# Kernel tuning notes

Measured on AMD Instinct MI355X. Metric: run time of the kernel, lower is better.

## Reference

```python
import jax, jax.numpy as jnp
import numpy as np

INP_SIZE = 3072
HID = 1024
OUT = 768
N_RES = 2  # same block (shared weights) applied twice, as in the torch code
EPS = 1e-5


def _layernorm(x, g, b):
    m = jnp.mean(x, axis=-1, keepdims=True)
    v = jnp.mean((x - m) ** 2, axis=-1, keepdims=True)
    return (x - m) / jnp.sqrt(v + EPS) * g + b


def setup_inputs() -> dict:
    key = jax.random.key(0)
    ks = jax.random.split(key, 8)
    bsz = 8192
    s = 0.02
    return {
        "inp": jax.random.normal(ks[0], (bsz, INP_SIZE), dtype=jnp.float32),
        "y": jax.random.normal(ks[1], (bsz, OUT), dtype=jnp.float32),
        "ln1_g": jnp.ones((INP_SIZE,), jnp.float32),
        "ln1_b": jnp.zeros((INP_SIZE,), jnp.float32),
        "W1": jax.random.normal(ks[2], (INP_SIZE, HID), dtype=jnp.float32) * s,
        "b1": jnp.zeros((HID,), jnp.float32),
        "Wa": jax.random.normal(ks[3], (HID, HID), dtype=jnp.float32) * s,
        "ba": jnp.zeros((HID,), jnp.float32),
        "Wb": jax.random.normal(ks[4], (HID, HID), dtype=jnp.float32) * s,
        "bb": jnp.zeros((HID,), jnp.float32),
        "W2": jax.random.normal(ks[5], (HID, OUT), dtype=jnp.float32) * s,
        "b2": jnp.zeros((OUT,), jnp.float32),
        "ln2_g": jnp.ones((OUT,), jnp.float32),
        "ln2_b": jnp.zeros((OUT,), jnp.float32),
    }


def reference(inp, y, ln1_g, ln1_b, W1, b1, Wa, ba, Wb, bb, W2, b2, ln2_g, ln2_b):
    bsz = inp.shape[0]
    # backbone (dropout in eval mode = identity)
    h = _layernorm(inp, ln1_g, ln1_b) @ W1 + b1  # [bsz, HID]
    for _ in range(N_RES):  # shared block weights, applied twice
        r = jax.nn.relu(jax.nn.relu(h @ Wa + ba) @ Wb + bb)
        h = h + r
    pred_y = _layernorm(h @ W2 + b2, ln2_g, ln2_b)  # [bsz, OUT]

    # batched contrastive cosine-sim loss (replaces per-sample python loop)
    pn = pred_y / jnp.linalg.norm(pred_y, axis=1, keepdims=True)
    yn = y / jnp.linalg.norm(y, axis=1, keepdims=True)
    S = pn @ yn.T  # [bsz, bsz] cosine similarities
    loss = -jnp.sum(pn * yn) + jnp.sum(jax.nn.logsumexp(S, axis=1))

    acc = jnp.mean((jnp.argmax(S, axis=1) == jnp.arange(bsz)).astype(jnp.float32))
    return pred_y, loss, acc
```

## Files before the change

### kernel.cpp

```cpp
#include <hip/hip_runtime.h>
#include <hip/hip_fp16.h>
#include <cstdint>
#include <math.h>

#define INP  3072
#define HID  1024
#define OUTD 768
#define BSZ  8192

typedef _Float16 f16;
typedef _Float16 f16x8 __attribute__((ext_vector_type(8)));
typedef _Float16 f16x4 __attribute__((ext_vector_type(4)));
typedef float    f32x4 __attribute__((ext_vector_type(4)));
typedef int      i32x4 __attribute__((ext_vector_type(4)));
typedef signed char s8;

static constexpr float LOG2E = 1.44269504088896340736f;
static constexpr float LN2   = 0.69314718055994530942f;
static constexpr float QS    = 384.0f;
static constexpr float CSC   = LOG2E / (QS * QS);

static constexpr size_t OFF_XH   = 0;
static constexpr size_t OFF_PN   = 0;
static constexpr size_t OFF_YN   = OFF_PN   + (size_t)BSZ*OUTD;
static constexpr size_t OFF_PSUM = OFF_YN   + (size_t)BSZ*OUTD;
static constexpr size_t OFF_PMAX = OFF_PSUM + (size_t)BSZ*64*4;
static constexpr size_t OFF_HB   = OFF_XH   + (size_t)BSZ*INP*2;
static constexpr size_t OFF_TT   = OFF_HB   + (size_t)BSZ*HID*2;
static constexpr size_t OFF_W1T  = OFF_TT   + (size_t)BSZ*OUTD*4;
static constexpr size_t OFF_WAT  = OFF_W1T  + (size_t)INP*HID*2;
static constexpr size_t OFF_WBT  = OFF_WAT  + (size_t)HID*HID*2;
static constexpr size_t OFF_W2T  = OFF_WBT  + (size_t)HID*HID*2;
static constexpr size_t OFF_DIAG = OFF_W2T  + (size_t)HID*OUTD*2;
static constexpr size_t OFF_ACC  = OFF_DIAG + (size_t)BSZ*4;

#define GL2LDS(gp, lp) __builtin_amdgcn_global_load_lds( \
    (__attribute__((address_space(1))) void*)(uintptr_t)(gp), \
    (__attribute__((address_space(3))) void*)(unsigned)(uintptr_t)(lp), 16, 0, 0)

__device__ __forceinline__ float blk_sum256(float v, float* sm) {
  #pragma unroll
  for (int d = 1; d < 64; d <<= 1) v += __shfl_xor(v, d, 64);
  int tid = threadIdx.x;
  __syncthreads();
  if ((tid & 63) == 0) sm[tid >> 6] = v;
  __syncthreads();
  return sm[0] + sm[1] + sm[2] + sm[3];
}

__device__ __forceinline__ s8 q8(float v) {
  int q = __float2int_rn(v * QS);
  q = q > 127 ? 127 : (q < -127 ? -127 : q);
  return (s8)q;
}

__global__ __launch_bounds__(256) void ln1_kernel(const float* __restrict__ inp,
    const float* __restrict__ g, const float* __restrict__ b, f16* __restrict__ xh) {
  __shared__ float sm[4];
  const int row = blockIdx.x, tid = threadIdx.x;
  const float4* x4 = (const float4*)(inp + (size_t)row * INP);
  float4 v[3]; float s = 0.f;
  #pragma unroll
  for (int i = 0; i < 3; i++) { v[i] = x4[tid + i*256]; s += v[i].x+v[i].y+v[i].z+v[i].w; }
  const float mean = blk_sum256(s, sm) * (1.f/INP);
  float s2 = 0.f;
  #pragma unroll
  for (int i = 0; i < 3; i++) {
    float dx=v[i].x-mean, dy=v[i].y-mean, dz=v[i].z-mean, dw=v[i].w-mean;
    s2 += dx*dx+dy*dy+dz*dz+dw*dw;
  }
  const float rstd = rsqrtf(blk_sum256(s2, sm) * (1.f/INP) + 1e-5f);
  const float4* g4p = (const float4*)g;
  const float4* b4p = (const float4*)b;
  f16x4* o4 = (f16x4*)(xh + (size_t)row * INP);
  #pragma unroll
  for (int i = 0; i < 3; i++) {
    const int c = tid + i*256;
    const float4 gg = g4p[c], bb = b4p[c];
    f16x4 t;
    t[0] = (f16)((v[i].x-mean)*rstd*gg.x + bb.x);
    t[1] = (f16)((v[i].y-mean)*rstd*gg.y + bb.y);
    t[2] = (f16)((v[i].z-mean)*rstd*gg.z + bb.z);
    t[3] = (f16)((v[i].w-mean)*rstd*gg.w + bb.w);
    o4[c] = t;
  }
}

__global__ __launch_bounds__(256) void transpose_all(
    const float* __restrict__ W1, const float* __restrict__ Wa,
    const float* __restrict__ Wb, const float* __restrict__ W2,
    f16* __restrict__ W1T, f16* __restrict__ WAT,
    f16* __restrict__ WBT, f16* __restrict__ W2T) {
  __shared__ float t[32][33];
  const int bI = blockIdx.x;
  const float* W; f16* Wt; int K, N, n0, k0;
  if (bI < 3072)      { int tt = bI;      W = W1; Wt = W1T; K = INP; N = HID;  n0 = (tt & 31)*32; k0 = (tt >> 5)*32; }
  else if (bI < 4096) { int tt = bI-3072; W = Wa; Wt = WAT; K = HID; N = HID;  n0 = (tt & 31)*32; k0 = (tt >> 5)*32; }
  else if (bI < 5120) { int tt = bI-4096; W = Wb; Wt = WBT; K = HID; N = HID;  n0 = (tt & 31)*32; k0 = (tt >> 5)*32; }
  else                { int tt = bI-5120; W = W2; Wt = W2T; K = HID; N = OUTD; int kq = tt/24; n0 = (tt - kq*24)*32; k0 = kq*32; }
  const int tx = threadIdx.x & 31, ty = threadIdx.x >> 5;
  #pragma unroll
  for (int i = 0; i < 32; i += 8) t[ty+i][tx] = W[(size_t)(k0+ty+i)*N + n0+tx];
  __syncthreads();
  #pragma unroll
  for (int i = 0; i < 32; i += 8) Wt[(size_t)(n0+ty+i)*K + k0+tx] = (f16)t[tx][ty+i];
}

__global__ __launch_bounds__(256) void ln2_yn(const float* __restrict__ pre,
    const float* __restrict__ g, const float* __restrict__ b,
    const float* __restrict__ y,
    float* __restrict__ outY, s8* __restrict__ pn, s8* __restrict__ yn) {
  __shared__ float sm[4];
  const int tid = threadIdx.x;
  if ((int)blockIdx.x < BSZ) {
    const int row = blockIdx.x;
    const float* x = pre + (size_t)row * OUTD;
    float v[3]; float s = 0.f;
    #pragma unroll
    for (int i = 0; i < 3; i++) { v[i] = x[tid + i*256]; s += v[i]; }
    const float mean = blk_sum256(s, sm) * (1.f/OUTD);
    float s2 = 0.f;
    #pragma unroll
    for (int i = 0; i < 3; i++) { float d = v[i]-mean; s2 += d*d; }
    const float rstd = rsqrtf(blk_sum256(s2, sm) * (1.f/OUTD) + 1e-5f);
    float z[3]; float n2 = 0.f;
    #pragma unroll
    for (int i = 0; i < 3; i++) { int c = tid + i*256; z[i] = (v[i]-mean)*rstd*g[c] + b[c]; n2 += z[i]*z[i]; }
    const float rn = rsqrtf(blk_sum256(n2, sm));
    float* oy = outY + (size_t)row * OUTD;
    s8*   op = pn   + (size_t)row * OUTD;
    #pragma unroll
    for (int i = 0; i < 3; i++) { int c = tid + i*256; oy[c] = z[i]; op[c] = q8(z[i]*rn); }
  } else {
    const int row = blockIdx.x - BSZ;
    const float* x = y + (size_t)row * OUTD;
    float v[3]; float n2 = 0.f;
    #pragma unroll
    for (int i = 0; i < 3; i++) { v[i] = x[tid + i*256]; n2 += v[i]*v[i]; }
    const float rn = rsqrtf(blk_sum256(n2, sm));
    s8* o = yn + (size_t)row * OUTD;
    #pragma unroll
    for (int i = 0; i < 3; i++) { int c = tid + i*256; o[c] = q8(v[i]*rn); }
  }
}

#define EPI_H   0
#define EPI_T   1
#define EPI_RES 2
#define EPI_P   3

template<int EPI>
__global__ __launch_bounds__(256) void gemm_bt(
    const f16* __restrict__ A, const f16* __restrict__ B, int K, int N,
    const float* __restrict__ bias, float* __restrict__ Cf, f16* __restrict__ Ch,
    const f16* __restrict__ Hin)
{
  __shared__ alignas(16) f16 lA[2][128*32];
  __shared__ alignas(16) f16 lB[2][128*32];
  const int tid  = threadIdx.x;
  const int wave = tid >> 6, lane = tid & 63;
  const int m0 = blockIdx.x * 128, n0 = blockIdx.y * 128;
  const int srow  = tid >> 2;
  const int skc   = tid & 3;
  const int skc_sw = skc ^ ((srow >> 1) & 3);
  const f16* gA = A + (size_t)(m0 + srow) * K + skc_sw*8;
  const f16* gB = B + (size_t)(n0 + srow) * K + skc_sw*8;
  const int wm = wave & 1, wn = wave >> 1;
  const int fm = lane & 15;
  const int g4 = lane >> 4;
  const int ks = (fm >> 1) & 3;
  const int ck = ((g4 ^ ks) * 8);

  f32x4 acc[4][4];
  #pragma unroll
  for (int i = 0; i < 4; i++)
    #pragma unroll
    for (int j = 0; j < 4; j++) acc[i][j] = (f32x4){0.f,0.f,0.f,0.f};

  const int iters = K >> 5;
  auto stage = [&](int buf, int k0) {
    f16* lAw = &lA[buf][wave*16*32];
    f16* lBw = &lB[buf][wave*16*32];
    GL2LDS(gA + k0,                lAw);
    GL2LDS(gA + (size_t)64*K + k0, lAw + 64*32);
    GL2LDS(gB + k0,                lBw);
    GL2LDS(gB + (size_t)64*K + k0, lBw + 64*32);
  };

  stage(0, 0);
  __syncthreads();
  for (int it = 0; it < iters; ++it) {
    const int cur = it & 1;
    if (it + 1 < iters) stage(cur ^ 1, (it + 1) << 5);
    f16x8 af[4], bf[4];
    #pragma unroll
    for (int i = 0; i < 4; i++) af[i] = *(const f16x8*)&lA[cur][(wm*64 + i*16 + fm)*32 + ck];
    #pragma unroll
    for (int j = 0; j < 4; j++) bf[j] = *(const f16x8*)&lB[cur][(wn*64 + j*16 + fm)*32 + ck];
    #pragma unroll
    for (int i = 0; i < 4; i++)
      #pragma unroll
      for (int j = 0; j < 4; j++)
        acc[i][j] = __builtin_amdgcn_mfma_f32_16x16x32_f16(af[i], bf[j], acc[i][j], 0, 0, 0);
    __syncthreads();
  }

  const int colb = n0 + wn*64;
  const int rowb = m0 + wm*64;
  #pragma unroll
  for (int i = 0; i < 4; i++) {
    #pragma unroll
    for (int j = 0; j < 4; j++) {
      const int col = colb + j*16 + fm;
      const float bs = bias[col];
      #pragma unroll
      for (int r = 0; r < 4; r++) {
        const int row = rowb + i*16 + g4*4 + r;
        float v = acc[i][j][r] + bs;
        const size_t idx = (size_t)row * N + col;
        if constexpr (EPI == EPI_H)        { Ch[idx] = (f16)v; }
        else if constexpr (EPI == EPI_T)   { v = fmaxf(v, 0.f); Ch[idx] = (f16)v; }
        else if constexpr (EPI == EPI_RES) { v = fmaxf(v, 0.f); v += (float)Hin[idx]; Ch[idx] = (f16)v; }
        else                               { Cf[idx] = v; }
      }
    }
  }
}

__global__ __launch_bounds__(256) void gemm_s8(
    const s8* __restrict__ A, const s8* __restrict__ B,
    float* __restrict__ partsum, float* __restrict__ partmax, float* __restrict__ diagv)
{
  __shared__ alignas(16) s8 lA[2][128*64];
  __shared__ alignas(16) s8 lB[2][128*64];
  __shared__ float redS[2][128], redM[2][128];
  const int K = OUTD;
  const int tid = threadIdx.x;
  const int wave = tid >> 6, lane = tid & 63;
  const int m0 = blockIdx.x * 128, n0 = blockIdx.y * 128;
  const int srow = tid >> 2;
  const int cl   = tid & 3;
  const int cg   = cl ^ ((srow ^ (srow >> 2)) & 3);
  const s8* gA = A + (size_t)(m0 + srow) * K + cg*16;
  const s8* gB = B + (size_t)(n0 + srow) * K + cg*16;
  const int wm = wave & 1, wn = wave >> 1;
  const int fm = lane & 15;
  const int g4 = lane >> 4;
  const int ksw = (fm ^ (fm >> 2)) & 3;
  const int ck8 = (g4 ^ ksw) * 16;

  i32x4 acc[4][4];
  #pragma unroll
  for (int i = 0; i < 4; i++)
    #pragma unroll
    for (int j = 0; j < 4; j++) acc[i][j] = (i32x4){0,0,0,0};

  auto stage = [&](int buf, int k0) {
    s8* lAw = &lA[buf][wave*16*64];
    s8* lBw = &lB[buf][wave*16*64];
    GL2LDS(gA + k0,                lAw);
    GL2LDS(gA + (size_t)64*K + k0, lAw + 64*64);
    GL2LDS(gB + k0,                lBw);
    GL2LDS(gB + (size_t)64*K + k0, lBw + 64*64);
  };

  stage(0, 0);
  __syncthreads();
  const int iters = K / 64;
  for (int it = 0; it < iters; ++it) {
    const int cur = it & 1;
    if (it + 1 < iters) stage(cur ^ 1, (it + 1) * 64);
    i32x4 af[4], bf[4];
    #pragma unroll
    for (int i = 0; i < 4; i++) af[i] = *(const i32x4*)&lA[cur][(wm*64 + i*16 + fm)*64 + ck8];
    #pragma unroll
    for (int j = 0; j < 4; j++) bf[j] = *(const i32x4*)&lB[cur][(wn*64 + j*16 + fm)*64 + ck8];
    #pragma unroll
    for (int i = 0; i < 4; i++)
      #pragma unroll
      for (int j = 0; j < 4; j++)
        acc[i][j] = __builtin_amdgcn_mfma_i32_16x16x64_i8(af[i], bf[j], acc[i][j], 0, 0, 0);
    __syncthreads();
  }

  if (m0 == n0) {
    #pragma unroll
    for (int i = 0; i < 4; i++)
      #pragma unroll
      for (int j = 0; j < 4; j++) {
        const int col = n0 + wn*64 + j*16 + fm;
        #pragma unroll
        for (int r = 0; r < 4; r++) {
          const int row = m0 + wm*64 + i*16 + g4*4 + r;
          if (row == col) diagv[row] = (float)acc[i][j][r] * CSC;
        }
      }
  }
  #pragma unroll
  for (int i = 0; i < 4; i++) {
    #pragma unroll
    for (int r = 0; r < 4; r++) {
      const float a0 = (float)acc[i][0][r] * CSC;
      const float a1 = (float)acc[i][1][r] * CSC;
      const float a2 = (float)acc[i][2][r] * CSC;
      const float a3 = (float)acc[i][3][r] * CSC;
      float s  = exp2f(a0) + exp2f(a1) + exp2f(a2) + exp2f(a3);
      float mx = fmaxf(fmaxf(a0, a1), fmaxf(a2, a3));
      #pragma unroll
      for (int d = 1; d < 16; d <<= 1) {
        s  += __shfl_xor(s, d, 64);
        mx  = fmaxf(mx, __shfl_xor(mx, d, 64));
      }
      if (fm == 0) { const int lrow = wm*64 + i*16 + g4*4 + r; redS[wn][lrow] = s; redM[wn][lrow] = mx; }
    }
  }
  __syncthreads();
  if (tid < 128) {
    const float sa = redS[0][tid] + redS[1][tid];
    const float ma = fmaxf(redM[0][tid], redM[1][tid]);
    const size_t p = (size_t)blockIdx.y * BSZ + m0 + tid;
    partsum[p] = sa; partmax[p] = ma;
  }
}

__global__ __launch_bounds__(256) void reduce_rows(const float* __restrict__ partsum,
    const float* __restrict__ partmax, const float* __restrict__ diagv,
    float* __restrict__ accum, float* __restrict__ out) {
  __shared__ float sm[4];
  const int row = blockIdx.x*256 + threadIdx.x;
  float s = 0.f, mx = -1e30f;
  for (int i = 0; i < 64; i++) {
    s  += partsum[(size_t)i*BSZ + row];
    mx  = fmaxf(mx, partmax[(size_t)i*BSZ + row]);
  }
  const float dgs  = diagv[row];
  const float corr = (dgs >= mx) ? 1.f : 0.f;
  const float lse  = logf(s);
  const float dg   = dgs * LN2;
  const float lse_s = blk_sum256(lse, sm);
  const float dg_s  = blk_sum256(dg, sm);
  const float c_s   = blk_sum256(corr, sm);
  if (threadIdx.x == 0) {
    atomicAdd(&accum[0], lse_s);
    atomicAdd(&accum[1], dg_s);
    atomicAdd(&accum[2], c_s);
    __threadfence();
    const unsigned old = atomicAdd((unsigned*)&accum[3], 1u);
    if (old == gridDim.x - 1) {
      const float a0 = atomicAdd(&accum[0], 0.f);
      const float a1 = atomicAdd(&accum[1], 0.f);
      const float a2 = atomicAdd(&accum[2], 0.f);
      out[0] = a0 - a1;
      out[1] = a2 * (1.f / BSZ);
    }
  }
}

extern "C" void kernel_launch(void* const* d_in, const int* in_sizes, int n_in,
                              void* d_out, int out_size, void* d_ws, size_t ws_size,
                              hipStream_t stream) {
  const float* inp  = (const float*)d_in[0];
  const float* y    = (const float*)d_in[1];
  const float* ln1g = (const float*)d_in[2];
  const float* ln1b = (const float*)d_in[3];
  const float* W1   = (const float*)d_in[4];
  const float* b1   = (const float*)d_in[5];
  const float* Wa   = (const float*)d_in[6];
  const float* ba   = (const float*)d_in[7];
  const float* Wb   = (const float*)d_in[8];
  const float* bb   = (const float*)d_in[9];
  const float* W2   = (const float*)d_in[10];
  const float* b2   = (const float*)d_in[11];
  const float* ln2g = (const float*)d_in[12];
  const float* ln2b = (const float*)d_in[13];
  float* out = (float*)d_out;

  char* ws = (char*)d_ws;
  f16*   XH   = (f16*)  (ws + OFF_XH);
  s8*    PN   = (s8*)   (ws + OFF_PN);
  s8*    YN   = (s8*)   (ws + OFF_YN);
  float* PSUM = (float*)(ws + OFF_PSUM);
  float* PMAX = (float*)(ws + OFF_PMAX);
  f16*   HB   = (f16*)  (ws + OFF_HB);
  f16*   T    = (f16*)  (ws + OFF_TT);
  float* PRE2 = (float*)(ws + OFF_TT);
  f16*   W1T  = (f16*)  (ws + OFF_W1T);
  f16*   WAT  = (f16*)  (ws + OFF_WAT);
  f16*   WBT  = (f16*)  (ws + OFF_WBT);
  f16*   W2T  = (f16*)  (ws + OFF_W2T);
  float* DIAG = (float*)(ws + OFF_DIAG);
  float* ACC  = (float*)(ws + OFF_ACC);

  transpose_all<<<5888, 256, 0, stream>>>(W1, Wa, Wb, W2, W1T, WAT, WBT, W2T);
  ln1_kernel<<<BSZ, 256, 0, stream>>>(inp, ln1g, ln1b, XH);

  gemm_bt<EPI_H><<<dim3(BSZ/128, HID/128), 256, 0, stream>>>(
      XH, W1T, INP, HID, b1, nullptr, HB, nullptr);

  for (int it = 0; it < 2; it++) {
    gemm_bt<EPI_T><<<dim3(BSZ/128, HID/128), 256, 0, stream>>>(
        HB, WAT, HID, HID, ba, nullptr, T, nullptr);
    gemm_bt<EPI_RES><<<dim3(BSZ/128, HID/128), 256, 0, stream>>>(
        T, WBT, HID, HID, bb, nullptr, HB, HB);
  }

  gemm_bt<EPI_P><<<dim3(BSZ/128, OUTD/128), 256, 0, stream>>>(
      HB, W2T, HID, OUTD, b2, PRE2, nullptr, nullptr);

  ln2_yn<<<2*BSZ, 256, 0, stream>>>(PRE2, ln2g, ln2b, y, out, PN, YN);

  hipMemsetAsync(ACC, 0, 4*sizeof(float), stream);

  gemm_s8<<<dim3(BSZ/128, BSZ/128), 256, 0, stream>>>(PN, YN, PSUM, PMAX, DIAG);

  reduce_rows<<<BSZ/256, 256, 0, stream>>>(PSUM, PMAX, DIAG, ACC, out + (size_t)BSZ*OUTD);
}
```

Before: 497.0 us.

## Pre-pack weights and int8 operands into MFMA fragment layout, load B directly to registers

Weights are transposed into an MFMA-fragment-packed layout, and the normalized int8 pred and target matrices are written in a packed 16-row tile layout. The GEMMs can then load B fragments (and both operands in the int8 similarity GEMM) straight from global memory into registers, bypassing LDS. The f16 GEMM now stages only A through LDS with a K=64 step and a new swizzle, and its grid axes are swapped. The int8 GEMM drops LDS staging entirely and remaps blocks so each XCD shares N tiles. This cuts LDS traffic and barriers, but relies on L2/cache hits for the direct global fragment loads, which are not coalesced the same way.

Result: slower. 543.9 us (+9.4%).

```diff
diff --git a/kernel.cpp b/kernel.cpp
--- a/kernel.cpp
+++ b/kernel.cpp
@@ -34,6 +34,7 @@
 static constexpr size_t OFF_DIAG = OFF_W2T  + (size_t)HID*OUTD*2;
 static constexpr size_t OFF_ACC  = OFF_DIAG + (size_t)BSZ*4;
 
+
 #define GL2LDS(gp, lp) __builtin_amdgcn_global_load_lds( \
     (__attribute__((address_space(1))) void*)(uintptr_t)(gp), \
     (__attribute__((address_space(3))) void*)(unsigned)(uintptr_t)(lp), 16, 0, 0)
@@ -86,7 +87,7 @@
   }
 }
 
-__global__ __launch_bounds__(256) void transpose_all(
+__global__ __launch_bounds__(256) void transpose_pack(
     const float* __restrict__ W1, const float* __restrict__ Wa,
     const float* __restrict__ Wb, const float* __restrict__ W2,
     f16* __restrict__ W1T, f16* __restrict__ WAT,
@@ -102,8 +103,17 @@
   #pragma unroll
   for (int i = 0; i < 32; i += 8) t[ty+i][tx] = W[(size_t)(k0+ty+i)*N + n0+tx];
   __syncthreads();
-  #pragma unroll
-  for (int i = 0; i < 32; i += 8) Wt[(size_t)(n0+ty+i)*K + k0+tx] = (f16)t[tx][ty+i];
+  const int tid = threadIdx.x;
+  if (tid < 128) {
+    const int fm = tid & 15, half = (tid >> 4) & 1, kc = tid >> 5;
+    const int n_l = half*16 + fm;
+    f16x8 v;
+    #pragma unroll
+    for (int e = 0; e < 8; e++) v[e] = (f16)t[kc*8 + e][n_l];
+    const int n_g = n0 + n_l;
+    const size_t off = ((size_t)(n_g >> 4)*(K >> 3) + (k0 >> 3) + kc)*128 + fm*8;
+    *(f16x8*)(Wt + off) = v;
+  }
 }
 
 __global__ __launch_bounds__(256) void ln2_yn(const float* __restrict__ pre,
@@ -128,9 +138,13 @@
     for (int i = 0; i < 3; i++) { int c = tid + i*256; z[i] = (v[i]-mean)*rstd*g[c] + b[c]; n2 += z[i]*z[i]; }
     const float rn = rsqrtf(blk_sum256(n2, sm));
     float* oy = outY + (size_t)row * OUTD;
-    s8*   op = pn   + (size_t)row * OUTD;
-    #pragma unroll
-    for (int i = 0; i < 3; i++) { int c = tid + i*256; oy[c] = z[i]; op[c] = q8(z[i]*rn); }
+    const size_t rbase = (size_t)(row >> 4)*48*256 + (row & 15)*16;
+    #pragma unroll
+    for (int i = 0; i < 3; i++) {
+      const int c = tid + i*256;
+      oy[c] = z[i];
+      pn[rbase + (size_t)(c >> 4)*256 + (c & 15)] = q8(z[i]*rn);
+    }
   } else {
     const int row = blockIdx.x - BSZ;
     const float* x = y + (size_t)row * OUTD;
@@ -138,9 +152,12 @@
     #pragma unroll
     for (int i = 0; i < 3; i++) { v[i] = x[tid + i*256]; n2 += v[i]*v[i]; }
     const float rn = rsqrtf(blk_sum256(n2, sm));
-    s8* o = yn + (size_t)row * OUTD;
-    #pragma unroll
-    for (int i = 0; i < 3; i++) { int c = tid + i*256; o[c] = q8(v[i]*rn); }
+    const size_t rbase = (size_t)(row >> 4)*48*256 + (row & 15)*16;
+    #pragma unroll
+    for (int i = 0; i < 3; i++) {
+      const int c = tid + i*256;
+      yn[rbase + (size_t)(c >> 4)*256 + (c & 15)] = q8(v[i]*rn);
+    }
   }
 }
 
@@ -151,25 +168,23 @@
 
 template<int EPI>
 __global__ __launch_bounds__(256) void gemm_bt(
-    const f16* __restrict__ A, const f16* __restrict__ B, int K, int N,
+    const f16* __restrict__ A, const f16* __restrict__ Bpk, int K, int N,
     const float* __restrict__ bias, float* __restrict__ Cf, f16* __restrict__ Ch,
     const f16* __restrict__ Hin)
 {
-  __shared__ alignas(16) f16 lA[2][128*32];
-  __shared__ alignas(16) f16 lB[2][128*32];
+  __shared__ alignas(16) f16 lA[2][128*64];
   const int tid  = threadIdx.x;
   const int wave = tid >> 6, lane = tid & 63;
-  const int m0 = blockIdx.x * 128, n0 = blockIdx.y * 128;
-  const int srow  = tid >> 2;
-  const int skc   = tid & 3;
-  const int skc_sw = skc ^ ((srow >> 1) & 3);
-  const f16* gA = A + (size_t)(m0 + srow) * K + skc_sw*8;
-  const f16* gB = B + (size_t)(n0 + srow) * K + skc_sw*8;
+  const int n0 = blockIdx.x * 128;
+  const int m0 = blockIdx.y * 128;
+  const int Kc = K >> 3;
+  const int sr8 = lane >> 3;
+  const int scg = (lane & 7) ^ sr8;
+  const f16* gA = A + (size_t)(m0 + wave*32 + sr8) * K + scg*8;
   const int wm = wave & 1, wn = wave >> 1;
   const int fm = lane & 15;
   const int g4 = lane >> 4;
-  const int ks = (fm >> 1) & 3;
-  const int ck = ((g4 ^ ks) * 8);
+  const f16* pB = Bpk + (size_t)lane * 8;
 
   f32x4 acc[4][4];
   #pragma unroll
@@ -177,31 +192,46 @@
     #pragma unroll
     for (int j = 0; j < 4; j++) acc[i][j] = (f32x4){0.f,0.f,0.f,0.f};
 
-  const int iters = K >> 5;
-  auto stage = [&](int buf, int k0) {
-    f16* lAw = &lA[buf][wave*16*32];
-    f16* lBw = &lB[buf][wave*16*32];
-    GL2LDS(gA + k0,                lAw);
-    GL2LDS(gA + (size_t)64*K + k0, lAw + 64*32);
-    GL2LDS(gB + k0,                lBw);
-    GL2LDS(gB + (size_t)64*K + k0, lBw + 64*32);
-  };
-
-  stage(0, 0);
+  auto stageA = [&](int buf, int it) {
+    f16* d = &lA[buf][wave*32*64];
+    const f16* g = gA + it*64;
+    #pragma unroll
+    for (int q = 0; q < 4; q++) GL2LDS(g + (size_t)q*8*K, d + q*8*64);
+  };
+  auto loadB = [&](f16x8 (*bf)[4], int it) {
+    #pragma unroll
+    for (int j = 0; j < 4; j++) {
+      const size_t nb = (size_t)(n0 >> 4) + wn*4 + j;
+      const f16* base = pB + (nb*Kc + (size_t)it*8)*128;
+      bf[0][j] = *(const f16x8*)(base);
+      bf[1][j] = *(const f16x8*)(base + 4*128);
+    }
+  };
+  auto computeStep = [&](const f16* lAc, f16x8 (*bf)[4]) {
+    #pragma unroll
+    for (int h = 0; h < 2; h++) {
+      f16x8 af[4];
+      #pragma unroll
+      for (int i = 0; i < 4; i++)
+        af[i] = *(const f16x8*)&lAc[(wm*64 + i*16 + fm)*64 + (((h*4+g4) ^ (fm & 7))*8)];
+      #pragma unroll
+      for (int i = 0; i < 4; i++)
+        #pragma unroll
+        for (int j = 0; j < 4; j++)
+          acc[i][j] = __builtin_amdgcn_mfma_f32_16x16x32_f16(af[i], bf[h][j], acc[i][j], 0, 0, 0);
+    }
+  };
+
+  f16x8 bfA[2][4], bfB[2][4];
+  const int iters = K >> 6;
+  stageA(0, 0); loadB(bfA, 0);
   __syncthreads();
-  for (int it = 0; it < iters; ++it) {
-    const int cur = it & 1;
-    if (it + 1 < iters) stage(cur ^ 1, (it + 1) << 5);
-    f16x8 af[4], bf[4];
-    #pragma unroll
-    for (int i = 0; i < 4; i++) af[i] = *(const f16x8*)&lA[cur][(wm*64 + i*16 + fm)*32 + ck];
-    #pragma unroll
-    for (int j = 0; j < 4; j++) bf[j] = *(const f16x8*)&lB[cur][(wn*64 + j*16 + fm)*32 + ck];
-    #pragma unroll
-    for (int i = 0; i < 4; i++)
-      #pragma unroll
-      for (int j = 0; j < 4; j++)
-        acc[i][j] = __builtin_amdgcn_mfma_f32_16x16x32_f16(af[i], bf[j], acc[i][j], 0, 0, 0);
+  for (int it = 0; it < iters; it += 2) {
+    if (it + 1 < iters) { stageA(1, it + 1); loadB(bfB, it + 1); }
+    computeStep(&lA[0][0], bfA);
+    __syncthreads();
+    if (it + 2 < iters) { stageA(0, it + 2); loadB(bfA, it + 2); }
+    computeStep(&lA[1][0], bfB);
     __syncthreads();
   }
 
@@ -228,26 +258,21 @@
 }
 
 __global__ __launch_bounds__(256) void gemm_s8(
-    const s8* __restrict__ A, const s8* __restrict__ B,
+    const s8* __restrict__ Apk, const s8* __restrict__ Bpk,
     float* __restrict__ partsum, float* __restrict__ partmax, float* __restrict__ diagv)
 {
-  __shared__ alignas(16) s8 lA[2][128*64];
-  __shared__ alignas(16) s8 lB[2][128*64];
   __shared__ float redS[2][128], redM[2][128];
-  const int K = OUTD;
   const int tid = threadIdx.x;
   const int wave = tid >> 6, lane = tid & 63;
-  const int m0 = blockIdx.x * 128, n0 = blockIdx.y * 128;
-  const int srow = tid >> 2;
-  const int cl   = tid & 3;
-  const int cg   = cl ^ ((srow ^ (srow >> 2)) & 3);
-  const s8* gA = A + (size_t)(m0 + srow) * K + cg*16;
-  const s8* gB = B + (size_t)(n0 + srow) * K + cg*16;
+  const int lin = blockIdx.x;
+  const int xcd = lin & 7, p = lin >> 3;
+  const int mb = p & 63, nb = (xcd << 3) + (p >> 6);
+  const int m0 = mb * 128, n0 = nb * 128;
   const int wm = wave & 1, wn = wave >> 1;
   const int fm = lane & 15;
   const int g4 = lane >> 4;
-  const int ksw = (fm ^ (fm >> 2)) & 3;
-  const int ck8 = (g4 ^ ksw) * 16;
+  const s8* pA = Apk + (size_t)lane * 16;
+  const s8* pB = Bpk + (size_t)lane * 16;
 
   i32x4 acc[4][4];
   #pragma unroll
@@ -255,35 +280,34 @@
     #pragma unroll
     for (int j = 0; j < 4; j++) acc[i][j] = (i32x4){0,0,0,0};
 
-  auto stage = [&](int buf, int k0) {
-    s8* lAw = &lA[buf][wave*16*64];
-    s8* lBw = &lB[buf][wave*16*64];
-    GL2LDS(gA + k0,                lAw);
-    GL2LDS(gA + (size_t)64*K + k0, lAw + 64*64);
-    GL2LDS(gB + k0,                lBw);
-    GL2LDS(gB + (size_t)64*K + k0, lBw + 64*64);
-  };
-
-  stage(0, 0);
-  __syncthreads();
-  const int iters = K / 64;
-  for (int it = 0; it < iters; ++it) {
-    const int cur = it & 1;
-    if (it + 1 < iters) stage(cur ^ 1, (it + 1) * 64);
-    i32x4 af[4], bf[4];
-    #pragma unroll
-    for (int i = 0; i < 4; i++) af[i] = *(const i32x4*)&lA[cur][(wm*64 + i*16 + fm)*64 + ck8];
-    #pragma unroll
-    for (int j = 0; j < 4; j++) bf[j] = *(const i32x4*)&lB[cur][(wn*64 + j*16 + fm)*64 + ck8];
+  auto loadA = [&](i32x4* af, int it) {
+    #pragma unroll
+    for (int i = 0; i < 4; i++)
+      af[i] = *(const i32x4*)(pA + ((size_t)(mb*8 + wm*4 + i)*48 + it*4)*256);
+  };
+  auto loadB = [&](i32x4* bf, int it) {
+    #pragma unroll
+    for (int j = 0; j < 4; j++)
+      bf[j] = *(const i32x4*)(pB + ((size_t)(nb*8 + wn*4 + j)*48 + it*4)*256);
+  };
+  auto mf = [&](i32x4* af, i32x4* bf) {
     #pragma unroll
     for (int i = 0; i < 4; i++)
       #pragma unroll
       for (int j = 0; j < 4; j++)
         acc[i][j] = __builtin_amdgcn_mfma_i32_16x16x64_i8(af[i], bf[j], acc[i][j], 0, 0, 0);
-    __syncthreads();
-  }
-
-  if (m0 == n0) {
+  };
+
+  i32x4 af0[4], bf0[4], af1[4], bf1[4];
+  loadA(af0, 0); loadB(bf0, 0);
+  for (int it = 0; it < 12; it += 2) {
+    loadA(af1, it + 1); loadB(bf1, it + 1);
+    mf(af0, bf0);
+    if (it + 2 < 12) { loadA(af0, it + 2); loadB(bf0, it + 2); }
+    mf(af1, bf1);
+  }
+
+  if (mb == nb) {
     #pragma unroll
     for (int i = 0; i < 4; i++)
       #pragma unroll
@@ -318,8 +342,8 @@
   if (tid < 128) {
     const float sa = redS[0][tid] + redS[1][tid];
     const float ma = fmaxf(redM[0][tid], redM[1][tid]);
-    const size_t p = (size_t)blockIdx.y * BSZ + m0 + tid;
-    partsum[p] = sa; partmax[p] = ma;
+    const size_t pidx = (size_t)nb * BSZ + m0 + tid;
+    partsum[pidx] = sa; partmax[pidx] = ma;
   }
 }
 
@@ -391,27 +415,27 @@
   float* DIAG = (float*)(ws + OFF_DIAG);
   float* ACC  = (float*)(ws + OFF_ACC);
 
-  transpose_all<<<5888, 256, 0, stream>>>(W1, Wa, Wb, W2, W1T, WAT, WBT, W2T);
+  transpose_pack<<<5888, 256, 0, stream>>>(W1, Wa, Wb, W2, W1T, WAT, WBT, W2T);
   ln1_kernel<<<BSZ, 256, 0, stream>>>(inp, ln1g, ln1b, XH);
 
-  gemm_bt<EPI_H><<<dim3(BSZ/128, HID/128), 256, 0, stream>>>(
+  gemm_bt<EPI_H><<<dim3(HID/128, BSZ/128), 256, 0, stream>>>(
       XH, W1T, INP, HID, b1, nullptr, HB, nullptr);
 
   for (int it = 0; it < 2; it++) {
-    gemm_bt<EPI_T><<<dim3(BSZ/128, HID/128), 256, 0, stream>>>(
+    gemm_bt<EPI_T><<<dim3(HID/128, BSZ/128), 256, 0, stream>>>(
         HB, WAT, HID, HID, ba, nullptr, T, nullptr);
-    gemm_bt<EPI_RES><<<dim3(BSZ/128, HID/128), 256, 0, stream>>>(
+    gemm_bt<EPI_RES><<<dim3(HID/128, BSZ/128), 256, 0, stream>>>(
         T, WBT, HID, HID, bb, nullptr, HB, HB);
   }
 
-  gemm_bt<EPI_P><<<dim3(BSZ/128, OUTD/128), 256, 0, stream>>>(
+  gemm_bt<EPI_P><<<dim3(OUTD/128, BSZ/128), 256, 0, stream>>>(
       HB, W2T, HID, OUTD, b2, PRE2, nullptr, nullptr);
 
   ln2_yn<<<2*BSZ, 256, 0, stream>>>(PRE2, ln2g, ln2b, y, out, PN, YN);
 
   hipMemsetAsync(ACC, 0, 4*sizeof(float), stream);
 
-  gemm_s8<<<dim3(BSZ/128, BSZ/128), 256, 0, stream>>>(PN, YN, PSUM, PMAX, DIAG);
+  gemm_s8<<<4096, 256, 0, stream>>>(PN, YN, PSUM, PMAX, DIAG);
 
   reduce_rows<<<BSZ/256, 256, 0, stream>>>(PSUM, PMAX, DIAG, ACC, out + (size_t)BSZ*OUTD);
 }
```
